# Kernel optimization log

Measured on AMD Instinct MI355X. Metric: run time of the kernel, lower is better.

## Reference

```python
import jax, jax.numpy as jnp
import numpy as np

F_NUM = 22528
L1, L2, L3 = 3072, 15, 32
COUNT = 8
PSQT = 8
MAXF = 32
B = 4096


def _select(stacked, ls_idx, out_features):
    # stacked: [B, COUNT*out_features] -> pick the bucket row per sample
    r = stacked.reshape(stacked.shape[0], COUNT, out_features)
    return jnp.take_along_axis(r, ls_idx[:, None, None], axis=1)[:, 0, :]


def setup_inputs() -> dict:
    key = jax.random.key(0)
    ks = jax.random.split(key, 16)
    D = L1 + PSQT
    inp = {
        'us': jax.random.uniform(ks[0], (B, 1), jnp.float32),
        'them': None,
        'white_indices': jax.random.randint(ks[1], (B, MAXF), 0, F_NUM),
        'white_values': jax.random.uniform(ks[2], (B, MAXF), jnp.float32),
        'black_indices': jax.random.randint(ks[3], (B, MAXF), 0, F_NUM),
        'black_values': jax.random.uniform(ks[4], (B, MAXF), jnp.float32),
        'psqt_indices': jax.random.randint(ks[5], (B,), 0, PSQT),
        'layer_stack_indices': jax.random.randint(ks[6], (B,), 0, COUNT),
    }
    inp['them'] = 1.0 - inp['us']
    # parameters
    inp['ft_weight'] = jax.random.normal(ks[7], (F_NUM, D), jnp.float32) * 0.01
    inp['ft_bias'] = jax.random.normal(ks[8], (D,), jnp.float32) * 0.01
    inp['l1_w'] = jax.random.normal(ks[9], (COUNT * (L2 + 1), L1), jnp.float32) * 0.02
    inp['l1_b'] = jax.random.normal(ks[10], (COUNT * (L2 + 1),), jnp.float32) * 0.02
    inp['l1f_w'] = jax.random.normal(ks[11], (L2 + 1, L1), jnp.float32) * 0.02
    inp['l1f_b'] = jax.random.normal(ks[12], (L2 + 1,), jnp.float32) * 0.02
    inp['l2_w'] = jax.random.normal(ks[13], (COUNT * L3, 2 * L2), jnp.float32) * 0.1
    inp['l2_b'] = jax.random.normal(ks[14], (COUNT * L3,), jnp.float32) * 0.1
    inp['out_w'] = jax.random.normal(ks[15], (COUNT * 1, L3), jnp.float32) * 0.1
    inp['out_b'] = jnp.zeros((COUNT * 1,), jnp.float32)
    return inp


def reference(us, them, white_indices, white_values, black_indices, black_values,
              psqt_indices, layer_stack_indices, ft_weight, ft_bias,
              l1_w, l1_b, l1f_w, l1f_b, l2_w, l2_b, out_w, out_b):
    # DoubleFeatureTransformerSlice: sparse embedding accumulation
    wp = jnp.einsum('bmd,bm->bd', ft_weight[white_indices], white_values) + ft_bias
    bp = jnp.einsum('bmd,bm->bd', ft_weight[black_indices], black_values) + ft_bias
    w, wpsqt = wp[:, :L1], wp[:, L1:]
    b, bpsqt = bp[:, :L1], bp[:, L1:]
    l0 = us * jnp.concatenate([w, b], 1) + them * jnp.concatenate([b, w], 1)
    l0 = jnp.clip(l0, 0.0, 1.0)
    h = L1 // 2
    s0, s1, s2, s3 = l0[:, :h], l0[:, h:2*h], l0[:, 2*h:3*h], l0[:, 3*h:]
    l0 = jnp.concatenate([s0 * s1, s2 * s3], 1) * (127.0 / 128.0)  # [B, L1]
    wps = jnp.take_along_axis(wpsqt, psqt_indices[:, None], axis=1)
    bps = jnp.take_along_axis(bpsqt, psqt_indices[:, None], axis=1)
    # LayerStacks (dense over all buckets, then gather)
    mw = l1_w + jnp.tile(l1f_w, (COUNT, 1))
    mb = l1_b + jnp.tile(l1f_b, (COUNT,))
    l1c = _select(l0 @ mw.T + mb, layer_stack_indices, L2 + 1)
    l1x, l1x_out = l1c[:, :L2], l1c[:, L2:]
    l1x = jnp.clip(jnp.concatenate([jnp.square(l1x) * (127.0 / 128.0), l1x], 1), 0.0, 1.0)
    l2c = _select(l1x @ l2_w.T + l2_b, layer_stack_indices, L3)
    l2x = jnp.clip(l2c, 0.0, 1.0)
    l3c = _select(l2x @ out_w.T + out_b, layer_stack_indices, 1)
    x = l3c + l1x_out
    return x + (wps - bps) * (us - 0.5)
```

## Files before the change

### kernel.cpp

```cpp
#include <hip/hip_runtime.h>
#include <hip/hip_fp16.h>


#define DTOT 3080
#define TBL16_BYTES 138772480ull
#define MW_BYTES    1572864ull

constexpr float kScale = 127.0f / 128.0f;

__device__ __forceinline__ float clip01(float x) { return fminf(fmaxf(x, 0.0f), 1.0f); }

__device__ __forceinline__ void fma4(float4& a, float s, const float4 v) {
    a.x += s * v.x; a.y += s * v.y; a.z += s * v.z; a.w += s * v.w;
}

__device__ __forceinline__ float4 mix_clip(float u, float th, const float4 w, const float4 b) {
    float4 r;
    r.x = clip01(u * w.x + th * b.x);
    r.y = clip01(u * w.y + th * b.y);
    r.z = clip01(u * w.z + th * b.z);
    r.w = clip01(u * w.w + th * b.w);
    return r;
}

__device__ __forceinline__ float4 mul_scale(const float4 a, const float4 b) {
    float4 r;
    r.x = a.x * b.x * kScale;
    r.y = a.y * b.y * kScale;
    r.z = a.z * b.z * kScale;
    r.w = a.w * b.w * kScale;
    return r;
}

__global__ __launch_bounds__(256) void convert_tbl(const unsigned long long* __restrict__ in,
                                                   uint2* __restrict__ out, int n4)
{
    union Un { unsigned long long u[2]; float f[4]; };
    union Pk { __half2 h2[2]; uint2 u2; };
    for (int i = blockIdx.x * 256 + threadIdx.x; i < n4; i += gridDim.x * 256) {
        Un v;
        v.u[0] = __builtin_nontemporal_load(&in[2 * (size_t)i]);
        v.u[1] = __builtin_nontemporal_load(&in[2 * (size_t)i + 1]);
        Pk p;
        p.h2[0] = __floats2half2_rn(v.f[0], v.f[1]);
        p.h2[1] = __floats2half2_rn(v.f[2], v.f[3]);
        out[i] = p.u2;
    }
}

__global__ __launch_bounds__(256) void merge_l1(const float* __restrict__ l1w,
                                                const float* __restrict__ l1fw,
                                                float* __restrict__ mw)
{
    const int idx = blockIdx.x * 256 + threadIdx.x;
    const float4* a = (const float4*)l1w;
    const float4* f = (const float4*)l1fw;
    float4* o = (float4*)mw;
    const int row = idx / 768;
    const int k = row & 15;
    const int col = idx - row * 768;
    const float4 x = a[idx];
    const float4 y = f[k * 768 + col];
    float4 r;
    r.x = x.x + y.x; r.y = x.y + y.y; r.z = x.z + y.z; r.w = x.w + y.w;
    o[idx] = r;
}

__global__ __launch_bounds__(512, 2) void nnue_fp16(
    const float* __restrict__ us_arr, const float* __restrict__ them_arr,
    const int* __restrict__ wi, const float* __restrict__ wv,
    const int* __restrict__ bi, const float* __restrict__ bv,
    const int* __restrict__ pidx, const int* __restrict__ lsidx,
    const __half* __restrict__ tbl, const float* __restrict__ ftb,
    const float* __restrict__ mw,
    const float* __restrict__ l1b, const float* __restrict__ l1fb,
    const float* __restrict__ l2w, const float* __restrict__ l2b,
    const float* __restrict__ ow, const float* __restrict__ ob,
    float* __restrict__ out)
{
    const int b = blockIdx.x;
    const int t = threadIdx.x;

    __shared__ float4 lds_acc[1540];
    __shared__ int   sidx[64];
    __shared__ float sval[64];
    __shared__ float red[4][16];
    __shared__ float l1c[16];
    __shared__ float l1x[30];

    if (t < 32)      { sidx[t] = wi[b * 32 + t];      sval[t] = wv[b * 32 + t]; }
    else if (t < 64) { sidx[t] = bi[b * 32 + t - 32]; sval[t] = bv[b * 32 + t - 32]; }

    for (int ph = 0; ph < 32; ++ph) {
        __syncthreads();
        if (t < 32) {
            const int half = t >> 4;
            const int k = t & 15;
            const int j = 2 * k + (ph & 1);
            if (j + 1 < 32) {
                const int a = half * 32 + j, c = a + 1;
                const int ia = sidx[a], ic = sidx[c];
                if (ia > ic) {
                    const float va = sval[a], vc = sval[c];
                    sidx[a] = ic; sidx[c] = ia;
                    sval[a] = vc; sval[c] = va;
                }
            }
        }
    }
    __syncthreads();

    const int u0 = t;
    const bool c0 = (u0 >= 385);
    const int p0 = c0 ? (u0 - 385) : u0;
    const bool has1 = (t < 258);
    const int p1 = t + 127;

    const float4* fb4 = (const float4*)ftb;
    float4 A0a = fb4[2 * p0], A0b = fb4[2 * p0 + 1];
    float4 A1a = has1 ? fb4[2 * p1] : float4{0.f, 0.f, 0.f, 0.f};
    float4 A1b = has1 ? fb4[2 * p1 + 1] : float4{0.f, 0.f, 0.f, 0.f};

    #pragma unroll 4
    for (int m = 0; m < 32; ++m) {
        const __half* rowW = tbl + (size_t)sidx[m]      * DTOT;
        const __half* rowB = tbl + (size_t)sidx[32 + m] * DTOT;
        const float vw = sval[m], vb = sval[32 + m];

        const float v0 = c0 ? vb : vw;
        const uint4 raw0 = ((const uint4*)(c0 ? rowB : rowW))[p0];
        const __half2* h0 = (const __half2*)&raw0;
        {
            const float2 q0 = __half22float2(h0[0]);
            const float2 q1 = __half22float2(h0[1]);
            const float2 q2 = __half22float2(h0[2]);
            const float2 q3 = __half22float2(h0[3]);
            A0a.x += v0 * q0.x; A0a.y += v0 * q0.y; A0a.z += v0 * q1.x; A0a.w += v0 * q1.y;
            A0b.x += v0 * q2.x; A0b.y += v0 * q2.y; A0b.z += v0 * q3.x; A0b.w += v0 * q3.y;
        }
        if (has1) {
            const uint4 raw1 = ((const uint4*)rowB)[p1];
            const __half2* h1 = (const __half2*)&raw1;
            const float2 q0 = __half22float2(h1[0]);
            const float2 q1 = __half22float2(h1[1]);
            const float2 q2 = __half22float2(h1[2]);
            const float2 q3 = __half22float2(h1[3]);
            A1a.x += vb * q0.x; A1a.y += vb * q0.y; A1a.z += vb * q1.x; A1a.w += vb * q1.y;
            A1b.x += vb * q2.x; A1b.y += vb * q2.y; A1b.z += vb * q3.x; A1b.w += vb * q3.y;
        }
    }

    {
        const int g0 = (c0 ? 770 : 0) + 2 * p0;
        lds_acc[g0] = A0a; lds_acc[g0 + 1] = A0b;
        if (has1) {
            const int g1 = 770 + 2 * p1;
            lds_acc[g1] = A1a; lds_acc[g1 + 1] = A1b;
        }
    }
    __syncthreads();

    const float usv = us_arr[b];
    const float thv = them_arr[b];
    const int ls = lsidx[b];

    const float4* mwbase = (const float4*)mw + (size_t)ls * 16 * 768;

    const int lane = t & 63;
    const int wave = t >> 6;

    if (t < 256) {
        float4 fvv[3];
        #pragma unroll
        for (int i = 0; i < 3; ++i) {
            const int col = t + 256 * i;
            const int q = (col >= 384) ? (col - 384) : col;
            const float4 W0 = lds_acc[q],       W1 = lds_acc[q + 384];
            const float4 B0 = lds_acc[770 + q], B1 = lds_acc[770 + q + 384];
            fvv[i] = (col >= 384)
                ? mul_scale(mix_clip(usv, thv, B0, W0), mix_clip(usv, thv, B1, W1))
                : mul_scale(mix_clip(usv, thv, W0, B0), mix_clip(usv, thv, W1, B1));
        }

        #pragma unroll
        for (int half = 0; half < 2; ++half) {
            float acc[8];
            #pragma unroll
            for (int k = 0; k < 8; ++k) acc[k] = 0.f;

            #pragma unroll
            for (int i = 0; i < 3; ++i) {
                const int col = t + 256 * i;
                const float4 fv = fvv[i];
                #pragma unroll
                for (int k = 0; k < 8; ++k) {
                    const float4 w1 = mwbase[(size_t)(half * 8 + k) * 768 + col];
                    acc[k] += fv.x * w1.x + fv.y * w1.y + fv.z * w1.z + fv.w * w1.w;
                }
            }

            #pragma unroll
            for (int k = 0; k < 8; ++k) {
                #pragma unroll
                for (int off = 32; off > 0; off >>= 1)
                    acc[k] += __shfl_xor(acc[k], off, 64);
            }
            if (lane == 0) {
                #pragma unroll
                for (int k = 0; k < 8; ++k) red[wave][half * 8 + k] = acc[k];
            }
        }
    }
    __syncthreads();

    if (t < 16) {
        l1c[t] = red[0][t] + red[1][t] + red[2][t] + red[3][t]
               + l1b[ls * 16 + t] + l1fb[t];
    }
    __syncthreads();

    if (t < 15) {
        const float v = l1c[t];
        l1x[t]      = clip01(v * v * kScale);
        l1x[15 + t] = clip01(v);
    }
    __syncthreads();

    float partial = 0.f;
    if (t < 32) {
        const float* r2 = l2w + (size_t)(ls * 32 + t) * 30;
        float s2 = l2b[ls * 32 + t];
        #pragma unroll
        for (int i = 0; i < 30; ++i) s2 += l1x[i] * r2[i];
        partial = clip01(s2) * ow[ls * 32 + t];
    }
    #pragma unroll
    for (int off = 16; off > 0; off >>= 1)
        partial += __shfl_xor(partial, off, 64);

    if (t == 0) {
        const int pi = pidx[b];
        const float* pw = (const float*)&lds_acc[768];
        const float* pb = (const float*)&lds_acc[770 + 768];
        out[b] = partial + ob[ls] + l1c[15]
               + (pw[pi] - pb[pi]) * (usv - 0.5f);
    }
}

__global__ __launch_bounds__(512, 2) void nnue_fused(
    const float* __restrict__ us_arr, const float* __restrict__ them_arr,
    const int* __restrict__ wi, const float* __restrict__ wv,
    const int* __restrict__ bi, const float* __restrict__ bv,
    const int* __restrict__ pidx, const int* __restrict__ lsidx,
    const float* __restrict__ ftw, const float* __restrict__ ftb,
    const float* __restrict__ l1w, const float* __restrict__ l1b,
    const float* __restrict__ l1fw, const float* __restrict__ l1fb,
    const float* __restrict__ l2w, const float* __restrict__ l2b,
    const float* __restrict__ ow, const float* __restrict__ ob,
    float* __restrict__ out)
{
    const int b = blockIdx.x;
    const int t = threadIdx.x;

    __shared__ float4 lds_acc[1540];
    __shared__ int   sidx[64];
    __shared__ float sval[64];
    __shared__ float red[4][16];
    __shared__ float l1c[16];
    __shared__ float l1x[30];

    if (t < 32)      { sidx[t] = wi[b * 32 + t];      sval[t] = wv[b * 32 + t]; }
    else if (t < 64) { sidx[t] = bi[b * 32 + t - 32]; sval[t] = bv[b * 32 + t - 32]; }
    __syncthreads();

    const int g0 = t, g1 = t + 512, g2 = t + 1024;
    const int c1 = (g1 >= 770);
    const int s0 = t;
    const int s1 = c1 ? (g1 - 770) : g1;
    const int s2 = g2 - 770;
    const bool has3 = (t < 4);
    const int s3 = 766 + t;

    const float4* fb4 = (const float4*)ftb;
    float4 a0 = fb4[s0], a1 = fb4[s1], a2 = fb4[s2];
    float4 a3 = has3 ? fb4[s3] : float4{0.f, 0.f, 0.f, 0.f};

    #pragma unroll 2
    for (int m = 0; m < 32; ++m) {
        const float4* rw = (const float4*)(ftw + (size_t)sidx[m]      * DTOT);
        const float4* rb = (const float4*)(ftw + (size_t)sidx[32 + m] * DTOT);
        const float vw = sval[m], vb = sval[32 + m];

        fma4(a0, vw, rw[s0]);
        const float4* p1 = c1 ? rb : rw;
        fma4(a1, c1 ? vb : vw, p1[s1]);
        fma4(a2, vb, rb[s2]);
        if (has3) fma4(a3, vb, rb[s3]);
    }

    lds_acc[g0] = a0;
    lds_acc[g1] = a1;
    lds_acc[g2] = a2;
    if (has3) lds_acc[1536 + t] = a3;
    __syncthreads();

    const float usv = us_arr[b];
    const float thv = them_arr[b];
    const int ls = lsidx[b];

    const float4* w1base = (const float4*)(l1w + (size_t)ls * 16 * 3072);
    const float4* w2base = (const float4*)l1fw;

    const int lane = t & 63;
    const int wave = t >> 6;

    if (t < 256) {
        float acc[16];
        #pragma unroll
        for (int k = 0; k < 16; ++k) acc[k] = 0.f;

        #pragma unroll
        for (int i = 0; i < 3; ++i) {
            const int col = t + 256 * i;
            const int q = (col >= 384) ? (col - 384) : col;
            const float4 W0 = lds_acc[q],       W1 = lds_acc[q + 384];
            const float4 B0 = lds_acc[770 + q], B1 = lds_acc[770 + q + 384];
            const float4 fv = (col >= 384)
                ? mul_scale(mix_clip(usv, thv, B0, W0), mix_clip(usv, thv, B1, W1))
                : mul_scale(mix_clip(usv, thv, W0, B0), mix_clip(usv, thv, W1, B1));
            #pragma unroll
            for (int k = 0; k < 16; ++k) {
                const float4 w1 = w1base[(size_t)k * 768 + col];
                const float4 w2 = w2base[(size_t)k * 768 + col];
                acc[k] += fv.x * (w1.x + w2.x) + fv.y * (w1.y + w2.y)
                        + fv.z * (w1.z + w2.z) + fv.w * (w1.w + w2.w);
            }
        }

        #pragma unroll
        for (int k = 0; k < 16; ++k) {
            #pragma unroll
            for (int off = 32; off > 0; off >>= 1)
                acc[k] += __shfl_xor(acc[k], off, 64);
        }
        if (lane == 0) {
            #pragma unroll
            for (int k = 0; k < 16; ++k) red[wave][k] = acc[k];
        }
    }
    __syncthreads();

    if (t < 16) {
        l1c[t] = red[0][t] + red[1][t] + red[2][t] + red[3][t]
               + l1b[ls * 16 + t] + l1fb[t];
    }
    __syncthreads();

    if (t < 15) {
        const float v = l1c[t];
        l1x[t]      = clip01(v * v * kScale);
        l1x[15 + t] = clip01(v);
    }
    __syncthreads();

    float partial = 0.f;
    if (t < 32) {
        const float* r2 = l2w + (size_t)(ls * 32 + t) * 30;
        float s2 = l2b[ls * 32 + t];
        #pragma unroll
        for (int i = 0; i < 30; ++i) s2 += l1x[i] * r2[i];
        partial = clip01(s2) * ow[ls * 32 + t];
    }
    #pragma unroll
    for (int off = 16; off > 0; off >>= 1)
        partial += __shfl_xor(partial, off, 64);

    if (t == 0) {
        const int pi = pidx[b];
        const float* pw = (const float*)&lds_acc[768];
        const float* pb = (const float*)&lds_acc[770 + 768];
        out[b] = partial + ob[ls] + l1c[15]
               + (pw[pi] - pb[pi]) * (usv - 0.5f);
    }
}

extern "C" void kernel_launch(void* const* d_in, const int* in_sizes, int n_in,
                              void* d_out, int out_size, void* d_ws, size_t ws_size,
                              hipStream_t stream) {
    const float* us   = (const float*)d_in[0];
    const float* them = (const float*)d_in[1];
    const int*   wi   = (const int*)d_in[2];
    const float* wv   = (const float*)d_in[3];
    const int*   bi   = (const int*)d_in[4];
    const float* bv   = (const float*)d_in[5];
    const int*   pidx = (const int*)d_in[6];
    const int*   ls   = (const int*)d_in[7];
    const float* ftw  = (const float*)d_in[8];
    const float* ftb  = (const float*)d_in[9];
    const float* l1w  = (const float*)d_in[10];
    const float* l1b  = (const float*)d_in[11];
    const float* l1fw = (const float*)d_in[12];
    const float* l1fb = (const float*)d_in[13];
    const float* l2w  = (const float*)d_in[14];
    const float* l2b  = (const float*)d_in[15];
    const float* ow   = (const float*)d_in[16];
    const float* ob   = (const float*)d_in[17];
    float* out = (float*)d_out;

    const int B = in_sizes[0];
    const size_t need = TBL16_BYTES + MW_BYTES;

    if (ws_size >= need) {
        __half* tbl16 = (__half*)d_ws;
        float*  mw    = (float*)((char*)d_ws + TBL16_BYTES);
        convert_tbl<<<2048, 256, 0, stream>>>((const unsigned long long*)ftw, (uint2*)d_ws, 17346560);
        merge_l1<<<384, 256, 0, stream>>>(l1w, l1fw, mw);
        nnue_fp16<<<B, 512, 0, stream>>>(us, them, wi, wv, bi, bv, pidx, ls,
                                         tbl16, ftb, mw, l1b, l1fb,
                                         l2w, l2b, ow, ob, out);
    } else {
        nnue_fused<<<B, 512, 0, stream>>>(us, them, wi, wv, bi, bv, pidx, ls,
                                          ftw, ftb, l1w, l1b, l1fw, l1fb,
                                          l2w, l2b, ow, ob, out);
    }
}
```

Measured before the change: 335.1 us.

## Split fused NNUE kernel into parallel gather and MLP kernels via workspace

The fused per-sample kernel is split in two. A gather kernel uses 8 small blocks per sample to accumulate the sparse feature rows into a global workspace, and a separate MLP kernel reads those accumulators to run the layer stacks. This is meant to raise parallelism and latency hiding for the gather phase, at the cost of writing and re-reading about 100 MB of fp32 accumulators and an extra launch. The index-sorting pass is also removed from the old fused path, which is now only a fallback.

```diff
diff --git a/kernel.cpp b/kernel.cpp
--- a/kernel.cpp
+++ b/kernel.cpp
@@ -30,6 +30,16 @@
     r.z = a.z * b.z * kScale;
     r.w = a.w * b.w * kScale;
     return r;
+}
+
+__device__ __forceinline__ void acc_unit(float4& Aa, float4& Ab, const uint4 raw, float v) {
+    const __half2* h = (const __half2*)&raw;
+    const float2 q0 = __half22float2(h[0]);
+    const float2 q1 = __half22float2(h[1]);
+    const float2 q2 = __half22float2(h[2]);
+    const float2 q3 = __half22float2(h[3]);
+    Aa.x += v * q0.x; Aa.y += v * q0.y; Aa.z += v * q1.x; Aa.w += v * q1.y;
+    Ab.x += v * q2.x; Ab.y += v * q2.y; Ab.z += v * q3.x; Ab.w += v * q3.y;
 }
 
 __global__ __launch_bounds__(256) void convert_tbl(const unsigned long long* __restrict__ in,
@@ -66,6 +76,147 @@
     o[idx] = r;
 }
 
+__global__ __launch_bounds__(128) void nnue_gather(
+    const int* __restrict__ wi, const float* __restrict__ wv,
+    const int* __restrict__ bi, const float* __restrict__ bv,
+    const __half* __restrict__ tbl, const float* __restrict__ ftb,
+    float4* __restrict__ acc_ws)
+{
+    const int blk = blockIdx.x;
+    const int b = blk >> 3;
+    const int s = blk & 7;
+    const int t = threadIdx.x;
+
+    __shared__ int   sidx[64];
+    __shared__ float sval[64];
+    if (t < 32)      { sidx[t] = wi[b * 32 + t];      sval[t] = wv[b * 32 + t]; }
+    else if (t < 64) { sidx[t] = bi[b * 32 + t - 32]; sval[t] = bv[b * 32 + t - 32]; }
+    __syncthreads();
+
+    const int lo = 96 * s + (s < 2 ? s : 2);
+    const int size = (s < 2) ? 97 : 96;
+    if (t >= size) return;
+
+    const int u = lo + t;
+    const bool cb = (u >= 385);
+    const int p = cb ? (u - 385) : u;
+
+    const float4* fb4 = (const float4*)ftb;
+    float4 Aa = fb4[2 * p], Ab = fb4[2 * p + 1];
+
+    #pragma unroll 4
+    for (int m = 0; m < 32; ++m) {
+        const int row = cb ? sidx[32 + m] : sidx[m];
+        const float v = cb ? sval[32 + m] : sval[m];
+        const uint4 raw = ((const uint4*)(tbl + (size_t)row * DTOT))[p];
+        acc_unit(Aa, Ab, raw, v);
+    }
+
+    float4* dst = acc_ws + ((size_t)b * 1540 + 2 * u);
+    dst[0] = Aa; dst[1] = Ab;
+}
+
+__global__ __launch_bounds__(256) void nnue_mlp(
+    const float* __restrict__ us_arr, const float* __restrict__ them_arr,
+    const int* __restrict__ pidx, const int* __restrict__ lsidx,
+    const float4* __restrict__ acc_ws, const float* __restrict__ mw,
+    const float* __restrict__ l1b, const float* __restrict__ l1fb,
+    const float* __restrict__ l2w, const float* __restrict__ l2b,
+    const float* __restrict__ ow, const float* __restrict__ ob,
+    float* __restrict__ out)
+{
+    const int b = blockIdx.x;
+    const int t = threadIdx.x;
+
+    __shared__ float red[4][16];
+    __shared__ float l1c[16];
+    __shared__ float l1x[30];
+
+    const float usv = us_arr[b];
+    const float thv = them_arr[b];
+    const int ls = lsidx[b];
+    const float4* acc = acc_ws + (size_t)b * 1540;
+    const float4* mwbase = (const float4*)mw + (size_t)ls * 16 * 768;
+
+    const int lane = t & 63;
+    const int wave = t >> 6;
+
+    float4 fvv[3];
+    #pragma unroll
+    for (int i = 0; i < 3; ++i) {
+        const int col = t + 256 * i;
+        const int q = (col >= 384) ? (col - 384) : col;
+        const float4 W0 = acc[q],       W1 = acc[q + 384];
+        const float4 B0 = acc[770 + q], B1 = acc[770 + q + 384];
+        fvv[i] = (col >= 384)
+            ? mul_scale(mix_clip(usv, thv, B0, W0), mix_clip(usv, thv, B1, W1))
+            : mul_scale(mix_clip(usv, thv, W0, B0), mix_clip(usv, thv, W1, B1));
+    }
+
+    #pragma unroll
+    for (int half = 0; half < 2; ++half) {
+        float acck[8];
+        #pragma unroll
+        for (int k = 0; k < 8; ++k) acck[k] = 0.f;
+
+        #pragma unroll
+        for (int i = 0; i < 3; ++i) {
+            const int col = t + 256 * i;
+            const float4 fv = fvv[i];
+            #pragma unroll
+            for (int k = 0; k < 8; ++k) {
+                const float4 w1 = mwbase[(size_t)(half * 8 + k) * 768 + col];
+                acck[k] += fv.x * w1.x + fv.y * w1.y + fv.z * w1.z + fv.w * w1.w;
+            }
+        }
+
+        #pragma unroll
+        for (int k = 0; k < 8; ++k) {
+            #pragma unroll
+            for (int off = 32; off > 0; off >>= 1)
+                acck[k] += __shfl_xor(acck[k], off, 64);
+        }
+        if (lane == 0) {
+            #pragma unroll
+            for (int k = 0; k < 8; ++k) red[wave][half * 8 + k] = acck[k];
+        }
+    }
+    __syncthreads();
+
+    if (t < 16) {
+        l1c[t] = red[0][t] + red[1][t] + red[2][t] + red[3][t]
+               + l1b[ls * 16 + t] + l1fb[t];
+    }
+    __syncthreads();
+
+    if (t < 15) {
+        const float v = l1c[t];
+        l1x[t]      = clip01(v * v * kScale);
+        l1x[15 + t] = clip01(v);
+    }
+    __syncthreads();
+
+    float partial = 0.f;
+    if (t < 32) {
+        const float* r2 = l2w + (size_t)(ls * 32 + t) * 30;
+        float s2 = l2b[ls * 32 + t];
+        #pragma unroll
+        for (int i = 0; i < 30; ++i) s2 += l1x[i] * r2[i];
+        partial = clip01(s2) * ow[ls * 32 + t];
+    }
+    #pragma unroll
+    for (int off = 16; off > 0; off >>= 1)
+        partial += __shfl_xor(partial, off, 64);
+
+    if (t == 0) {
+        const int pi = pidx[b];
+        const float* pw = (const float*)(acc + 768);
+        const float* pb = (const float*)(acc + 1538);
+        out[b] = partial + ob[ls] + l1c[15]
+               + (pw[pi] - pb[pi]) * (usv - 0.5f);
+    }
+}
+
 __global__ __launch_bounds__(512, 2) void nnue_fp16(
     const float* __restrict__ us_arr, const float* __restrict__ them_arr,
     const int* __restrict__ wi, const float* __restrict__ wv,
@@ -90,24 +241,6 @@
 
     if (t < 32)      { sidx[t] = wi[b * 32 + t];      sval[t] = wv[b * 32 + t]; }
     else if (t < 64) { sidx[t] = bi[b * 32 + t - 32]; sval[t] = bv[b * 32 + t - 32]; }
-
-    for (int ph = 0; ph < 32; ++ph) {
-        __syncthreads();
-        if (t < 32) {
-            const int half = t >> 4;
-            const int k = t & 15;
-            const int j = 2 * k + (ph & 1);
-            if (j + 1 < 32) {
-                const int a = half * 32 + j, c = a + 1;
-                const int ia = sidx[a], ic = sidx[c];
-                if (ia > ic) {
-                    const float va = sval[a], vc = sval[c];
-                    sidx[a] = ic; sidx[c] = ia;
-                    sval[a] = vc; sval[c] = va;
-                }
-            }
-        }
-    }
     __syncthreads();
 
     const int u0 = t;
@@ -129,24 +262,10 @@
 
         const float v0 = c0 ? vb : vw;
         const uint4 raw0 = ((const uint4*)(c0 ? rowB : rowW))[p0];
-        const __half2* h0 = (const __half2*)&raw0;
-        {
-            const float2 q0 = __half22float2(h0[0]);
-            const float2 q1 = __half22float2(h0[1]);
-            const float2 q2 = __half22float2(h0[2]);
-            const float2 q3 = __half22float2(h0[3]);
-            A0a.x += v0 * q0.x; A0a.y += v0 * q0.y; A0a.z += v0 * q1.x; A0a.w += v0 * q1.y;
-            A0b.x += v0 * q2.x; A0b.y += v0 * q2.y; A0b.z += v0 * q3.x; A0b.w += v0 * q3.y;
-        }
+        acc_unit(A0a, A0b, raw0, v0);
         if (has1) {
             const uint4 raw1 = ((const uint4*)rowB)[p1];
-            const __half2* h1 = (const __half2*)&raw1;
-            const float2 q0 = __half22float2(h1[0]);
-            const float2 q1 = __half22float2(h1[1]);
-            const float2 q2 = __half22float2(h1[2]);
-            const float2 q3 = __half22float2(h1[3]);
-            A1a.x += vb * q0.x; A1a.y += vb * q0.y; A1a.z += vb * q1.x; A1a.w += vb * q1.y;
-            A1b.x += vb * q2.x; A1b.y += vb * q2.y; A1b.z += vb * q3.x; A1b.w += vb * q3.y;
+            acc_unit(A1a, A1b, raw1, vb);
         }
     }
 
@@ -163,7 +282,6 @@
     const float usv = us_arr[b];
     const float thv = them_arr[b];
     const int ls = lsidx[b];
-
     const float4* mwbase = (const float4*)mw + (size_t)ls * 16 * 768;
 
     const int lane = t & 63;
@@ -184,9 +302,9 @@
 
         #pragma unroll
         for (int half = 0; half < 2; ++half) {
-            float acc[8];
-            #pragma unroll
-            for (int k = 0; k < 8; ++k) acc[k] = 0.f;
+            float acck[8];
+            #pragma unroll
+            for (int k = 0; k < 8; ++k) acck[k] = 0.f;
 
             #pragma unroll
             for (int i = 0; i < 3; ++i) {
@@ -195,7 +313,7 @@
                 #pragma unroll
                 for (int k = 0; k < 8; ++k) {
                     const float4 w1 = mwbase[(size_t)(half * 8 + k) * 768 + col];
-                    acc[k] += fv.x * w1.x + fv.y * w1.y + fv.z * w1.z + fv.w * w1.w;
+                    acck[k] += fv.x * w1.x + fv.y * w1.y + fv.z * w1.z + fv.w * w1.w;
                 }
             }
 
@@ -203,11 +321,11 @@
             for (int k = 0; k < 8; ++k) {
                 #pragma unroll
                 for (int off = 32; off > 0; off >>= 1)
-                    acc[k] += __shfl_xor(acc[k], off, 64);
+                    acck[k] += __shfl_xor(acck[k], off, 64);
             }
             if (lane == 0) {
                 #pragma unroll
-                for (int k = 0; k < 8; ++k) red[wave][half * 8 + k] = acc[k];
+                for (int k = 0; k < 8; ++k) red[wave][half * 8 + k] = acck[k];
             }
         }
     }
@@ -408,9 +526,20 @@
     float* out = (float*)d_out;
 
     const int B = in_sizes[0];
-    const size_t need = TBL16_BYTES + MW_BYTES;
-
-    if (ws_size >= need) {
+    const size_t acc_bytes = (size_t)B * 1540 * 16;
+    const size_t need_fp16 = TBL16_BYTES + MW_BYTES;
+    const size_t need_full = need_fp16 + acc_bytes;
+
+    if (ws_size >= need_full) {
+        __half* tbl16 = (__half*)d_ws;
+        float*  mw    = (float*)((char*)d_ws + TBL16_BYTES);
+        float4* accw  = (float4*)((char*)d_ws + TBL16_BYTES + MW_BYTES);
+        convert_tbl<<<2048, 256, 0, stream>>>((const unsigned long long*)ftw, (uint2*)d_ws, 17346560);
+        merge_l1<<<384, 256, 0, stream>>>(l1w, l1fw, mw);
+        nnue_gather<<<B * 8, 128, 0, stream>>>(wi, wv, bi, bv, tbl16, ftb, accw);
+        nnue_mlp<<<B, 256, 0, stream>>>(us, them, pidx, ls, accw, mw,
+                                        l1b, l1fb, l2w, l2b, ow, ob, out);
+    } else if (ws_size >= need_fp16) {
         __half* tbl16 = (__half*)d_ws;
         float*  mw    = (float*)((char*)d_ws + TBL16_BYTES);
         convert_tbl<<<2048, 256, 0, stream>>>((const unsigned long long*)ftw, (uint2*)d_ws, 17346560);
```

New measurement: 349.3 us. +4.3%, slower.
